# Optimization experiments

Measured on AMD Instinct MI355X. Metric: run time of the kernel, lower is better.

The kernel has to match this reference:

```python
import jax, jax.numpy as jnp
import numpy as np

N_DETS = 50000
DEG = 32
N_EDGES = N_DETS * DEG

def _xavier(key, fan_in, fan_out):
    lim = np.sqrt(6.0 / (fan_in + fan_out)).astype(np.float32)
    return jax.random.uniform(key, (fan_in, fan_out), jnp.float32, -lim, lim)

def setup_inputs() -> dict:
    key = jax.random.key(0)
    ks = jax.random.split(key, 10)
    detFeatures = jax.random.normal(ks[0], (N_DETS, 128), jnp.float32)
    # every detection has exactly DEG neighbor pairs -> sorted segment ids, no empty segments
    cIdxs = jnp.repeat(jnp.arange(N_DETS, dtype=jnp.int64), DEG)
    nIdxs = jax.random.randint(ks[1], (N_EDGES,), 0, N_DETS, jnp.int64)
    pairFeatures = jax.random.normal(ks[2], (N_EDGES, 32), jnp.float32)
    return {
        "detFeatures": detFeatures,
        "cIdxs": cIdxs,
        "nIdxs": nIdxs,
        "pairFeatures": pairFeatures,
        "W_fc1": _xavier(ks[3], 128, 32), "b_fc1": jnp.zeros((32,), jnp.float32),
        "W_pw1": _xavier(ks[4], 96, 64), "b_pw1": jnp.zeros((64,), jnp.float32),
        "W_pw2": _xavier(ks[5], 64, 64), "b_pw2": jnp.zeros((64,), jnp.float32),
        "W_pm1": _xavier(ks[6], 64, 64), "b_pm1": jnp.zeros((64,), jnp.float32),
        "W_pm2": _xavier(ks[7], 64, 64), "b_pm2": jnp.zeros((64,), jnp.float32),
        "W_out": _xavier(ks[8], 64, 128), "b_out": jnp.zeros((128,), jnp.float32),
    }

def reference(detFeatures, cIdxs, nIdxs, pairFeatures,
              W_fc1, b_fc1, W_pw1, b_pw1, W_pw2, b_pw2,
              W_pm1, b_pm1, W_pm2, b_pm2, W_out, b_out):
    relu = jax.nn.relu
    # fc1: [N,128] -> [N,32]
    h = relu(detFeatures @ W_fc1 + b_fc1)
    # gather center / neighbor feats per pair; zero neighbor feats on identity rows
    cFeats = h[cIdxs]                                   # [E,32]
    nFeats = jnp.where((cIdxs == nIdxs)[:, None], 0.0, h[nIdxs])  # [E,32]
    x = jnp.concatenate((pairFeatures, cFeats, nFeats), axis=1)   # [E,96]
    x = relu(x @ W_pw1 + b_pw1)                         # [E,64]
    x = relu(x @ W_pw2 + b_pw2)                         # [E,64]
    # per-detection segment max (replaces the O(N) python loop)
    m = jax.ops.segment_max(x, cIdxs, num_segments=detFeatures.shape[0])  # [N,64]
    m = relu(m @ W_pm1 + b_pm1)
    m = relu(m @ W_pm2 + b_pm2)
    refined = m @ W_out + b_out                         # [N,128]
    return relu(detFeatures + refined)
```

## Files before the change

kernel.cpp:

```cpp
#include <hip/hip_runtime.h>

#define NDET 50000
#define DEG 32
#define NEDGE (NDET * DEG)
#define NGROUP (NEDGE / 64)

typedef __attribute__((ext_vector_type(8))) short short8;
typedef __attribute__((ext_vector_type(4))) float f32x4;

__device__ inline unsigned short f2bf(float x) {
    unsigned int u = __builtin_bit_cast(unsigned int, x);
    unsigned int r = (u + 0x7FFFu + ((u >> 16) & 1u)) >> 16;
    return (unsigned short)r;
}

__device__ inline short8 pack8(float4 a, float4 b) {
    short8 r;
    r[0] = (short)f2bf(a.x); r[1] = (short)f2bf(a.y);
    r[2] = (short)f2bf(a.z); r[3] = (short)f2bf(a.w);
    r[4] = (short)f2bf(b.x); r[5] = (short)f2bf(b.y);
    r[6] = (short)f2bf(b.z); r[7] = (short)f2bf(b.w);
    return r;
}

__global__ __launch_bounds__(256) void fc1_kernel(
    const float* __restrict__ detF,
    const float* __restrict__ W,
    const float* __restrict__ b,
    unsigned short* __restrict__ hbf)
{
    __shared__ float Ws[128 * 32];
    for (int i = threadIdx.x; i < 128 * 32; i += 256) Ws[i] = W[i];
    __syncthreads();

    const int c = threadIdx.x & 31;
    const float bc = b[c];
    const int NG = NDET / 8;
    for (int rg = blockIdx.x; rg < NG; rg += (int)gridDim.x) {
        const int row = rg * 8 + (threadIdx.x >> 5);
        const float4* df4 = (const float4*)(detF + (size_t)row * 128);
        float acc = bc;
#pragma unroll
        for (int i = 0; i < 32; i++) {
            float4 d = df4[i];
            acc += d.x * Ws[(4 * i + 0) * 32 + c];
            acc += d.y * Ws[(4 * i + 1) * 32 + c];
            acc += d.z * Ws[(4 * i + 2) * 32 + c];
            acc += d.w * Ws[(4 * i + 3) * 32 + c];
        }
        hbf[(size_t)row * 32 + c] = f2bf(fmaxf(acc, 0.0f));
    }
}

__global__ __launch_bounds__(256, 2) void edge_kernel(
    const unsigned short* __restrict__ hbf,
    const int* __restrict__ nIdx,
    const float* __restrict__ pairF,
    const float* __restrict__ W1,
    const float* __restrict__ b1,
    const float* __restrict__ W2,
    const float* __restrict__ b2,
    unsigned short* __restrict__ m_bf)
{
    __shared__ __align__(16) unsigned short lds[4][64 * 72];

    const int tid  = threadIdx.x;
    const int lane = tid & 63;
    const int wv   = tid >> 6;
    const int m16  = lane & 15;
    const int q    = lane >> 4;

    unsigned short* st = &lds[0][0];
    for (int i = tid; i < 64 * 96; i += 256) {
        int n = i / 96, k = i - n * 96;
        st[i] = f2bf(W1[k * 64 + n]);
    }
    for (int i = tid; i < 64 * 64; i += 256) {
        int n = i >> 6, k = i & 63;
        st[6144 + i] = f2bf(W2[k * 64 + n]);
    }
    __syncthreads();

    short8 w1f[3][4];
#pragma unroll
    for (int nt = 0; nt < 4; nt++) {
        const unsigned short* base = &st[(nt * 16 + m16) * 96];
        w1f[0][nt] = *(const short8*)&base[q * 8];
        w1f[1][nt] = *(const short8*)&base[64 + q * 8];
        w1f[2][nt] = *(const short8*)&base[32 + q * 8];
    }
    float b1r[4], b2r[4];
#pragma unroll
    for (int nt = 0; nt < 4; nt++) {
        b1r[nt] = b1[nt * 16 + m16];
        b2r[nt] = b2[nt * 16 + m16];
    }
    __syncthreads();

    unsigned short* Y1w = &lds[wv][0];
    const unsigned short* W2T = nullptr;
    (void)W2T;
    short8 w2f[2][4];
#pragma unroll
    for (int nt = 0; nt < 4; nt++) {
        w2f[0][nt] = *(const short8*)&st[6144 + (nt * 16 + m16) * 64 + q * 8];
        w2f[1][nt] = *(const short8*)&st[6144 + (nt * 16 + m16) * 64 + 32 + q * 8];
    }
    __syncthreads();

    const int wstride = (int)gridDim.x * 4;
    int g = blockIdx.x * 4 + wv;
    if (g >= NGROUP) return;

    int    ni[4];
    float4 pv[4][2];
    short8 nb[4];
    short8 cf2[2];

#define PREF(gg)                                                                  \
    {                                                                             \
        const int E0p = (gg) * 64, d0p = (gg) * 2;                                \
        _Pragma("unroll")                                                         \
        for (int mt = 0; mt < 4; mt++) {                                          \
            int e = E0p + mt * 16 + m16;                                          \
            ni[mt] = nIdx[e];                                                     \
            const float* pr = pairF + (size_t)e * 32 + q * 8;                     \
            pv[mt][0] = *(const float4*)pr;                                       \
            pv[mt][1] = *(const float4*)(pr + 4);                                 \
            nb[mt] = *(const short8*)&hbf[(size_t)ni[mt] * 32 + q * 8];           \
        }                                                                         \
        cf2[0] = *(const short8*)&hbf[(size_t)d0p * 32 + q * 8];                  \
        cf2[1] = *(const short8*)&hbf[(size_t)(d0p + 1) * 32 + q * 8];            \
    }

    PREF(g);
    const short8 zr = {0, 0, 0, 0, 0, 0, 0, 0};

    while (true) {
        const int d0 = g * 2;
        short8 ap[4], an[4], ac[4];
#pragma unroll
        for (int mt = 0; mt < 4; mt++) {
            ap[mt] = pack8(pv[mt][0], pv[mt][1]);
            an[mt] = (ni[mt] == d0 + (mt >> 1)) ? zr : nb[mt];
            ac[mt] = cf2[mt >> 1];
        }
        const int gn = g + wstride;
        const bool more = (gn < NGROUP);
        PREF(more ? gn : g);

        f32x4 acc[4][4];
#pragma unroll
        for (int mt = 0; mt < 4; mt++)
#pragma unroll
            for (int nt = 0; nt < 4; nt++) {
                float c0 = b1r[nt];
                acc[mt][nt] = (f32x4){c0, c0, c0, c0};
            }
#pragma unroll
        for (int mt = 0; mt < 4; mt++)
#pragma unroll
            for (int nt = 0; nt < 4; nt++) {
                acc[mt][nt] = __builtin_amdgcn_mfma_f32_16x16x32_bf16(ap[mt], w1f[0][nt], acc[mt][nt], 0, 0, 0);
                acc[mt][nt] = __builtin_amdgcn_mfma_f32_16x16x32_bf16(an[mt], w1f[1][nt], acc[mt][nt], 0, 0, 0);
                acc[mt][nt] = __builtin_amdgcn_mfma_f32_16x16x32_bf16(ac[mt], w1f[2][nt], acc[mt][nt], 0, 0, 0);
            }

#pragma unroll
        for (int mt = 0; mt < 4; mt++)
#pragma unroll
            for (int nt = 0; nt < 4; nt++)
#pragma unroll
                for (int r = 0; r < 4; r++)
                    Y1w[(mt * 16 + q * 4 + r) * 72 + nt * 16 + m16] =
                        f2bf(fmaxf(acc[mt][nt][r], 0.0f));

        f32x4 acc2[4][4];
#pragma unroll
        for (int mt = 0; mt < 4; mt++)
#pragma unroll
            for (int nt = 0; nt < 4; nt++) {
                float c0 = b2r[nt];
                acc2[mt][nt] = (f32x4){c0, c0, c0, c0};
            }
#pragma unroll
        for (int ks = 0; ks < 2; ks++) {
            short8 af[4];
#pragma unroll
            for (int mt = 0; mt < 4; mt++)
                af[mt] = *(const short8*)&Y1w[(mt * 16 + m16) * 72 + ks * 32 + q * 8];
#pragma unroll
            for (int mt = 0; mt < 4; mt++)
#pragma unroll
                for (int nt = 0; nt < 4; nt++)
                    acc2[mt][nt] = __builtin_amdgcn_mfma_f32_16x16x32_bf16(af[mt], w2f[ks][nt], acc2[mt][nt], 0, 0, 0);
        }

#pragma unroll
        for (int d = 0; d < 2; d++)
#pragma unroll
            for (int nt = 0; nt < 4; nt++) {
                float v = 0.0f;
#pragma unroll
                for (int mt = 2 * d; mt < 2 * d + 2; mt++)
#pragma unroll
                    for (int r = 0; r < 4; r++) v = fmaxf(v, acc2[mt][nt][r]);
                v = fmaxf(v, __shfl_xor(v, 16));
                v = fmaxf(v, __shfl_xor(v, 32));
                if (q == 0) m_bf[(size_t)(d0 + d) * 64 + nt * 16 + m16] = f2bf(v);
            }

        if (!more) break;
        g = gn;
    }
#undef PREF
}

__global__ __launch_bounds__(256, 2) void tail_kernel(
    const float* __restrict__ detF,
    const unsigned short* __restrict__ m_bf,
    const float* __restrict__ Wm1, const float* __restrict__ bm1,
    const float* __restrict__ Wm2, const float* __restrict__ bm2,
    const float* __restrict__ Wo,  const float* __restrict__ bo,
    float* __restrict__ out)
{
    __shared__ __align__(16) unsigned short W1T[64 * 72];
    __shared__ __align__(16) unsigned short W2T[64 * 72];
    __shared__ __align__(16) unsigned short WoT[128 * 72];
    __shared__ __align__(16) unsigned short Tt[4][64 * 72];

    const int tid  = threadIdx.x;
    const int lane = tid & 63;
    const int wv   = tid >> 6;
    const int m16  = lane & 15;
    const int q    = lane >> 4;

    for (int i = tid; i < 64 * 64; i += 256) {
        int n = i >> 6, k = i & 63;
        W1T[n * 72 + k] = f2bf(Wm1[k * 64 + n]);
        W2T[n * 72 + k] = f2bf(Wm2[k * 64 + n]);
    }
    for (int i = tid; i < 128 * 64; i += 256) {
        int n = i >> 6, k = i & 63;
        WoT[n * 72 + k] = f2bf(Wo[k * 128 + n]);
    }
    __syncthreads();

    float bm1r[4], bm2r[4], bor[8];
#pragma unroll
    for (int nt = 0; nt < 4; nt++) {
        bm1r[nt] = bm1[nt * 16 + m16];
        bm2r[nt] = bm2[nt * 16 + m16];
    }
#pragma unroll
    for (int nt = 0; nt < 8; nt++) bor[nt] = bo[nt * 16 + m16];

    unsigned short* Tw = &Tt[wv][0];
    const int NTG = (NDET + 63) / 64;

    for (int gI = blockIdx.x * 4 + wv; gI < NTG; gI += (int)gridDim.x * 4) {
        const int d0 = gI * 64;

        f32x4 acc[4][4];
#pragma unroll
        for (int mt = 0; mt < 4; mt++)
#pragma unroll
            for (int nt = 0; nt < 4; nt++) {
                float c0 = bm1r[nt];
                acc[mt][nt] = (f32x4){c0, c0, c0, c0};
            }
#pragma unroll
        for (int ks = 0; ks < 2; ks++) {
            short8 af[4];
#pragma unroll
            for (int mt = 0; mt < 4; mt++) {
                int row = d0 + mt * 16 + m16;
                if (row >= NDET) row = NDET - 1;
                af[mt] = *(const short8*)&m_bf[(size_t)row * 64 + ks * 32 + q * 8];
            }
#pragma unroll
            for (int mt = 0; mt < 4; mt++)
#pragma unroll
                for (int nt = 0; nt < 4; nt++) {
                    short8 bf = *(const short8*)&W1T[(nt * 16 + m16) * 72 + ks * 32 + q * 8];
                    acc[mt][nt] = __builtin_amdgcn_mfma_f32_16x16x32_bf16(af[mt], bf, acc[mt][nt], 0, 0, 0);
                }
        }
#pragma unroll
        for (int mt = 0; mt < 4; mt++)
#pragma unroll
            for (int nt = 0; nt < 4; nt++)
#pragma unroll
                for (int r = 0; r < 4; r++)
                    Tw[(mt * 16 + q * 4 + r) * 72 + nt * 16 + m16] =
                        f2bf(fmaxf(acc[mt][nt][r], 0.0f));

#pragma unroll
        for (int mt = 0; mt < 4; mt++)
#pragma unroll
            for (int nt = 0; nt < 4; nt++) {
                float c0 = bm2r[nt];
                acc[mt][nt] = (f32x4){c0, c0, c0, c0};
            }
#pragma unroll
        for (int ks = 0; ks < 2; ks++) {
            short8 af[4];
#pragma unroll
            for (int mt = 0; mt < 4; mt++)
                af[mt] = *(const short8*)&Tw[(mt * 16 + m16) * 72 + ks * 32 + q * 8];
#pragma unroll
            for (int mt = 0; mt < 4; mt++)
#pragma unroll
                for (int nt = 0; nt < 4; nt++) {
                    short8 bf = *(const short8*)&W2T[(nt * 16 + m16) * 72 + ks * 32 + q * 8];
                    acc[mt][nt] = __builtin_amdgcn_mfma_f32_16x16x32_bf16(af[mt], bf, acc[mt][nt], 0, 0, 0);
                }
        }
#pragma unroll
        for (int mt = 0; mt < 4; mt++)
#pragma unroll
            for (int nt = 0; nt < 4; nt++)
#pragma unroll
                for (int r = 0; r < 4; r++)
                    Tw[(mt * 16 + q * 4 + r) * 72 + nt * 16 + m16] =
                        f2bf(fmaxf(acc[mt][nt][r], 0.0f));

        short8 a3[4][2];
#pragma unroll
        for (int ks = 0; ks < 2; ks++)
#pragma unroll
            for (int mt = 0; mt < 4; mt++)
                a3[mt][ks] = *(const short8*)&Tw[(mt * 16 + m16) * 72 + ks * 32 + q * 8];

#pragma unroll
        for (int h2 = 0; h2 < 2; h2++) {
            f32x4 acc3[4][4];
#pragma unroll
            for (int mt = 0; mt < 4; mt++)
#pragma unroll
                for (int nt = 0; nt < 4; nt++) {
                    float c0 = bor[h2 * 4 + nt];
                    acc3[mt][nt] = (f32x4){c0, c0, c0, c0};
                }
#pragma unroll
            for (int ks = 0; ks < 2; ks++)
#pragma unroll
                for (int mt = 0; mt < 4; mt++)
#pragma unroll
                    for (int nt = 0; nt < 4; nt++) {
                        short8 bf = *(const short8*)&WoT[((h2 * 4 + nt) * 16 + m16) * 72 + ks * 32 + q * 8];
                        acc3[mt][nt] = __builtin_amdgcn_mfma_f32_16x16x32_bf16(a3[mt][ks], bf, acc3[mt][nt], 0, 0, 0);
                    }
#pragma unroll
            for (int mt = 0; mt < 4; mt++)
#pragma unroll
                for (int r = 0; r < 4; r++) {
                    int row = d0 + mt * 16 + q * 4 + r;
                    if (row < NDET) {
#pragma unroll
                        for (int nt = 0; nt < 4; nt++) {
                            int col = (h2 * 4 + nt) * 16 + m16;
                            float v = detF[(size_t)row * 128 + col] + acc3[mt][nt][r];
                            out[(size_t)row * 128 + col] = fmaxf(v, 0.0f);
                        }
                    }
                }
        }
    }
}

extern "C" void kernel_launch(void* const* d_in, const int* in_sizes, int n_in,
                              void* d_out, int out_size, void* d_ws, size_t ws_size,
                              hipStream_t stream)
{
    const float* detF  = (const float*)d_in[0];
    const int*   nIdx  = (const int*)d_in[2];
    const float* pairF = (const float*)d_in[3];
    const float* W_fc1 = (const float*)d_in[4];
    const float* b_fc1 = (const float*)d_in[5];
    const float* W_pw1 = (const float*)d_in[6];
    const float* b_pw1 = (const float*)d_in[7];
    const float* W_pw2 = (const float*)d_in[8];
    const float* b_pw2 = (const float*)d_in[9];
    const float* W_pm1 = (const float*)d_in[10];
    const float* b_pm1 = (const float*)d_in[11];
    const float* W_pm2 = (const float*)d_in[12];
    const float* b_pm2 = (const float*)d_in[13];
    const float* W_out = (const float*)d_in[14];
    const float* b_out = (const float*)d_in[15];
    float* out = (float*)d_out;

    unsigned short* hbf  = (unsigned short*)d_ws;
    unsigned short* m_bf = hbf + (size_t)NDET * 32;

    fc1_kernel<<<1024, 256, 0, stream>>>(detF, W_fc1, b_fc1, hbf);
    edge_kernel<<<1024, 256, 0, stream>>>(hbf, nIdx, pairF,
                                          W_pw1, b_pw1, W_pw2, b_pw2, m_bf);
    tail_kernel<<<256, 256, 0, stream>>>(detF, m_bf, W_pm1, b_pm1, W_pm2, b_pm2,
                                         W_out, b_out, out);
}
```

Measured before the change: 463.9 us.

## Use MFMA for fc1, move W2 fragments to LDS, raise edge occupancy

```diff
diff --git a/kernel.cpp b/kernel.cpp
--- a/kernel.cpp
+++ b/kernel.cpp
@@ -9,9 +9,7 @@
 typedef __attribute__((ext_vector_type(4))) float f32x4;
 
 __device__ inline unsigned short f2bf(float x) {
-    unsigned int u = __builtin_bit_cast(unsigned int, x);
-    unsigned int r = (u + 0x7FFFu + ((u >> 16) & 1u)) >> 16;
-    return (unsigned short)r;
+    return (unsigned short)((__builtin_bit_cast(unsigned int, x) + 0x8000u) >> 16);
 }
 
 __device__ inline short8 pack8(float4 a, float4 b) {
@@ -23,36 +21,68 @@
     return r;
 }
 
-__global__ __launch_bounds__(256) void fc1_kernel(
+__global__ __launch_bounds__(256, 4) void fc1_kernel(
     const float* __restrict__ detF,
     const float* __restrict__ W,
     const float* __restrict__ b,
     unsigned short* __restrict__ hbf)
 {
-    __shared__ float Ws[128 * 32];
-    for (int i = threadIdx.x; i < 128 * 32; i += 256) Ws[i] = W[i];
+    __shared__ __align__(16) unsigned short WT[32 * 136];
+
+    const int tid  = threadIdx.x;
+    const int lane = tid & 63;
+    const int wv   = tid >> 6;
+    const int m16  = lane & 15;
+    const int q    = lane >> 4;
+
+    for (int i = tid; i < 32 * 128; i += 256) {
+        int n = i >> 7, k = i & 127;
+        WT[n * 136 + k] = f2bf(W[k * 32 + n]);
+    }
     __syncthreads();
 
-    const int c = threadIdx.x & 31;
-    const float bc = b[c];
-    const int NG = NDET / 8;
-    for (int rg = blockIdx.x; rg < NG; rg += (int)gridDim.x) {
-        const int row = rg * 8 + (threadIdx.x >> 5);
-        const float4* df4 = (const float4*)(detF + (size_t)row * 128);
-        float acc = bc;
-#pragma unroll
-        for (int i = 0; i < 32; i++) {
-            float4 d = df4[i];
-            acc += d.x * Ws[(4 * i + 0) * 32 + c];
-            acc += d.y * Ws[(4 * i + 1) * 32 + c];
-            acc += d.z * Ws[(4 * i + 2) * 32 + c];
-            acc += d.w * Ws[(4 * i + 3) * 32 + c];
-        }
-        hbf[(size_t)row * 32 + c] = f2bf(fmaxf(acc, 0.0f));
-    }
-}
-
-__global__ __launch_bounds__(256, 2) void edge_kernel(
+    const int g = blockIdx.x * 4 + wv;
+    if (g >= (NDET + 63) / 64) return;
+    const int d0 = g * 64;
+
+    f32x4 acc[4][2];
+#pragma unroll
+    for (int nt = 0; nt < 2; nt++) {
+        float c0 = b[nt * 16 + m16];
+#pragma unroll
+        for (int mt = 0; mt < 4; mt++) acc[mt][nt] = (f32x4){c0, c0, c0, c0};
+    }
+
+#pragma unroll
+    for (int ks = 0; ks < 4; ks++) {
+#pragma unroll
+        for (int mt = 0; mt < 4; mt++) {
+            int row = d0 + mt * 16 + m16;
+            if (row >= NDET) row = NDET - 1;
+            const float* pr = detF + (size_t)row * 128 + ks * 32 + q * 8;
+            short8 a = pack8(*(const float4*)pr, *(const float4*)(pr + 4));
+#pragma unroll
+            for (int nt = 0; nt < 2; nt++) {
+                short8 bf = *(const short8*)&WT[(nt * 16 + m16) * 136 + ks * 32 + q * 8];
+                acc[mt][nt] = __builtin_amdgcn_mfma_f32_16x16x32_bf16(a, bf, acc[mt][nt], 0, 0, 0);
+            }
+        }
+    }
+
+#pragma unroll
+    for (int mt = 0; mt < 4; mt++)
+#pragma unroll
+        for (int r = 0; r < 4; r++) {
+            int row = d0 + mt * 16 + q * 4 + r;
+            if (row < NDET) {
+#pragma unroll
+                for (int nt = 0; nt < 2; nt++)
+                    hbf[(size_t)row * 32 + nt * 16 + m16] = f2bf(fmaxf(acc[mt][nt][r], 0.0f));
+            }
+        }
+}
+
+__global__ __launch_bounds__(256, 3) void edge_kernel(
     const unsigned short* __restrict__ hbf,
     const int* __restrict__ nIdx,
     const float* __restrict__ pairF,
@@ -62,7 +92,8 @@
     const float* __restrict__ b2,
     unsigned short* __restrict__ m_bf)
 {
-    __shared__ __align__(16) unsigned short lds[4][64 * 72];
+    __shared__ __align__(16) unsigned short Y1s[4][64 * 72];
+    __shared__ __align__(16) unsigned short W2T[64 * 72];
 
     const int tid  = threadIdx.x;
     const int lane = tid & 63;
@@ -70,14 +101,14 @@
     const int m16  = lane & 15;
     const int q    = lane >> 4;
 
-    unsigned short* st = &lds[0][0];
+    unsigned short* st = &Y1s[0][0];
     for (int i = tid; i < 64 * 96; i += 256) {
         int n = i / 96, k = i - n * 96;
         st[i] = f2bf(W1[k * 64 + n]);
     }
     for (int i = tid; i < 64 * 64; i += 256) {
         int n = i >> 6, k = i & 63;
-        st[6144 + i] = f2bf(W2[k * 64 + n]);
+        W2T[n * 72 + k] = f2bf(W2[k * 64 + n]);
     }
     __syncthreads();
 
@@ -97,16 +128,7 @@
     }
     __syncthreads();
 
-    unsigned short* Y1w = &lds[wv][0];
-    const unsigned short* W2T = nullptr;
-    (void)W2T;
-    short8 w2f[2][4];
-#pragma unroll
-    for (int nt = 0; nt < 4; nt++) {
-        w2f[0][nt] = *(const short8*)&st[6144 + (nt * 16 + m16) * 64 + q * 8];
-        w2f[1][nt] = *(const short8*)&st[6144 + (nt * 16 + m16) * 64 + 32 + q * 8];
-    }
-    __syncthreads();
+    unsigned short* Y1w = &Y1s[wv][0];
 
     const int wstride = (int)gridDim.x * 4;
     int g = blockIdx.x * 4 + wv;
@@ -190,10 +212,12 @@
             for (int mt = 0; mt < 4; mt++)
                 af[mt] = *(const short8*)&Y1w[(mt * 16 + m16) * 72 + ks * 32 + q * 8];
 #pragma unroll
-            for (int mt = 0; mt < 4; mt++)
-#pragma unroll
-                for (int nt = 0; nt < 4; nt++)
-                    acc2[mt][nt] = __builtin_amdgcn_mfma_f32_16x16x32_bf16(af[mt], w2f[ks][nt], acc2[mt][nt], 0, 0, 0);
+            for (int nt = 0; nt < 4; nt++) {
+                short8 wf = *(const short8*)&W2T[(nt * 16 + m16) * 72 + ks * 32 + q * 8];
+#pragma unroll
+                for (int mt = 0; mt < 4; mt++)
+                    acc2[mt][nt] = __builtin_amdgcn_mfma_f32_16x16x32_bf16(af[mt], wf, acc2[mt][nt], 0, 0, 0);
+            }
         }
 
 #pragma unroll
@@ -393,9 +417,9 @@
     unsigned short* hbf  = (unsigned short*)d_ws;
     unsigned short* m_bf = hbf + (size_t)NDET * 32;
 
-    fc1_kernel<<<1024, 256, 0, stream>>>(detF, W_fc1, b_fc1, hbf);
-    edge_kernel<<<1024, 256, 0, stream>>>(hbf, nIdx, pairF,
-                                          W_pw1, b_pw1, W_pw2, b_pw2, m_bf);
+    fc1_kernel<<<(NDET + 255) / 256, 256, 0, stream>>>(detF, W_fc1, b_fc1, hbf);
+    edge_kernel<<<768, 256, 0, stream>>>(hbf, nIdx, pairF,
+                                         W_pw1, b_pw1, W_pw2, b_pw2, m_bf);
     tail_kernel<<<256, 256, 0, stream>>>(detF, m_bf, W_pm1, b_pm1, W_pm2, b_pm2,
                                          W_out, b_out, out);
 }
```

Measured after the change: 458.7 us. About the same (-1.1%).
